# Performance work log

Measured on AMD Instinct MI355X. Metric: run time of the kernel, lower is better.

## Reference

```python
import jax, jax.numpy as jnp
import numpy as np

D_MODEL = 1024
N_HEAD = 16
HEAD_SIZE = D_MODEL // N_HEAD
SEQ = 2048
BATCH = 4
LN_EPS = 1e-5


def layer_norm(x, gamma, beta):
    mu = jnp.mean(x, axis=-1, keepdims=True)
    var = jnp.var(x, axis=-1, keepdims=True)
    return (x - mu) * jax.lax.rsqrt(var + LN_EPS) * gamma + beta


def setup_inputs() -> dict:
    key = jax.random.key(0)
    ks = jax.random.split(key, 12)
    s = 0.02
    return {
        "x": jax.random.normal(ks[0], (BATCH, SEQ, D_MODEL), jnp.float32),
        "Wq": jax.random.normal(ks[1], (N_HEAD, D_MODEL, HEAD_SIZE), jnp.float32) * s,
        "Wk": jax.random.normal(ks[2], (N_HEAD, D_MODEL, HEAD_SIZE), jnp.float32) * s,
        "Wv": jax.random.normal(ks[3], (N_HEAD, D_MODEL, HEAD_SIZE), jnp.float32) * s,
        "Wo": jax.random.normal(ks[4], (D_MODEL, D_MODEL), jnp.float32) * s,
        "bo": jnp.zeros((D_MODEL,), jnp.float32),
        "W1": jax.random.normal(ks[5], (D_MODEL, 4 * D_MODEL), jnp.float32) * s,
        "b1": jnp.zeros((4 * D_MODEL,), jnp.float32),
        "W2": jax.random.normal(ks[6], (4 * D_MODEL, D_MODEL), jnp.float32) * s,
        "b2": jnp.zeros((D_MODEL,), jnp.float32),
        "g1": jnp.ones((D_MODEL,), jnp.float32),
        "be1": jnp.zeros((D_MODEL,), jnp.float32),
        "g2": jnp.ones((D_MODEL,), jnp.float32),
        "be2": jnp.zeros((D_MODEL,), jnp.float32),
    }


def reference(x, Wq, Wk, Wv, Wo, bo, W1, b1, W2, b2, g1, be1, g2, be2):
    B, T, C = x.shape
    # --- self-attention branch (dropout = eval identity) ---
    h = layer_norm(x, g1, be1)
    q = jnp.einsum('btc,hcs->bhts', h, Wq)
    k = jnp.einsum('btc,hcs->bhts', h, Wk)
    v = jnp.einsum('btc,hcs->bhts', h, Wv)
    wei = jnp.einsum('bhts,bhus->bhtu', q, k) * (HEAD_SIZE ** -0.5)
    # non-standard diagonal mask: scores on the diagonal are set to 0 (not -inf)
    diag = jnp.eye(T, dtype=bool)
    wei = jnp.where(diag, jnp.zeros((), wei.dtype), wei)
    wei = jax.nn.softmax(wei, axis=-1)
    att = jnp.einsum('bhtu,bhus->bhts', wei, v)          # [B,H,T,hs]
    att = att.transpose(0, 2, 1, 3).reshape(B, T, C)      # concat heads
    sa = att @ Wo + bo
    x = x + sa
    # --- feed-forward branch ---
    h2 = layer_norm(x, g2, be2)
    ff = jax.nn.gelu(h2 @ W1 + b1, approximate=False) @ W2 + b2
    return x + ff
```

## Files before the change

kernel.cpp:

```cpp
#include <hip/hip_runtime.h>
#include <hip/hip_bf16.h>
#include <math.h>

#define D_MODEL 1024
#define N_HEAD 16
#define HEAD 64
#define SEQ 2048
#define BATCH 4
#define ROWS (BATCH*SEQ)
#define FFD 4096

typedef __bf16 bf16;
typedef __attribute__((ext_vector_type(8))) __bf16 bf16x8;
typedef __attribute__((ext_vector_type(4))) __bf16 bf16x4;
typedef __attribute__((ext_vector_type(4))) float f32x4;
typedef __attribute__((ext_vector_type(16))) float f32x16;
typedef __attribute__((ext_vector_type(4))) short short4v;

static_assert(sizeof(bf16x8) == 16, "bf16x8 must be 16B");

__device__ __forceinline__ void async_copy16(const void* g, void* l) {
  __builtin_amdgcn_global_load_lds((const __attribute__((address_space(1))) void*)g,
                                   (__attribute__((address_space(3))) void*)l, 16, 0, 0);
}

__device__ __forceinline__ f32x4 mfma16(bf16x8 a, bf16x8 b, f32x4 c) {
  return __builtin_amdgcn_mfma_f32_16x16x32_bf16(a, b, c, 0, 0, 0);
}

__device__ __forceinline__ f32x16 mfma32(bf16x8 a, bf16x8 b, f32x16 c) {
  return __builtin_amdgcn_mfma_f32_32x32x16_bf16(a, b, c, 0, 0, 0);
}

__device__ __forceinline__ f32x4 mfma16k16(bf16x4 a, bf16x4 b, f32x4 c) {
#if __has_builtin(__builtin_amdgcn_mfma_f32_16x16x16_bf16)
  return __builtin_amdgcn_mfma_f32_16x16x16_bf16(a, b, c, 0, 0, 0);
#else
  return __builtin_amdgcn_mfma_f32_16x16x16bf16_1k(__builtin_bit_cast(short4v, a),
                                                   __builtin_bit_cast(short4v, b), c, 0, 0, 0);
#endif
}

__device__ __forceinline__ float fast_exp2(float x) {
#if __has_builtin(__builtin_amdgcn_exp2f)
  return __builtin_amdgcn_exp2f(x);
#else
  float r; asm("v_exp_f32 %0, %1" : "=v"(r) : "v"(x)); return r;
#endif
}

__device__ __forceinline__ float fast_gelu(float x) {
  const float y = 0.7978845608f * (x + 0.044715f * x * x * x);
  const float e = fast_exp2(y * 2.88539008178f);
  return 0.5f * x * (1.f + (1.f - 2.f / (e + 1.f)));
}

__global__ __launch_bounds__(256) void transpose_cast_kernel(const float* __restrict__ in,
                                                             bf16* __restrict__ out,
                                                             int R, int C) {
  __shared__ float ts[32][33];
  const int r0 = blockIdx.y * 32, c0 = blockIdx.x * 32;
  const int t = threadIdx.x, lr = t >> 3, lc = (t & 7) * 4;
  const float4 v = *(const float4*)(in + (size_t)(r0 + lr) * C + c0 + lc);
  ts[lr][lc + 0] = v.x; ts[lr][lc + 1] = v.y; ts[lr][lc + 2] = v.z; ts[lr][lc + 3] = v.w;
  __syncthreads();
  bf16x4 o;
  o[0] = (bf16)ts[lc + 0][lr]; o[1] = (bf16)ts[lc + 1][lr];
  o[2] = (bf16)ts[lc + 2][lr]; o[3] = (bf16)ts[lc + 3][lr];
  *(bf16x4*)(out + (size_t)(c0 + lr) * R + r0 + lc) = o;
}

__global__ __launch_bounds__(256) void qkv_transpose_kernel(const float* __restrict__ Wq,
                                                            const float* __restrict__ Wk,
                                                            const float* __restrict__ Wv,
                                                            bf16* __restrict__ out) {
  __shared__ float ts[32][33];
  const int mat = blockIdx.z / N_HEAD, h = blockIdx.z % N_HEAD;
  const float* W = (mat == 0 ? Wq : mat == 1 ? Wk : Wv) + (size_t)h * D_MODEL * HEAD;
  bf16* o = out + (size_t)mat * D_MODEL * D_MODEL + (size_t)(h * HEAD) * D_MODEL;
  const int c0 = blockIdx.x * 32, s0 = blockIdx.y * 32;
  const int t = threadIdx.x, lr = t >> 3, lc = (t & 7) * 4;
  const float4 v = *(const float4*)(W + (size_t)(c0 + lr) * HEAD + s0 + lc);
  ts[lr][lc + 0] = v.x; ts[lr][lc + 1] = v.y; ts[lr][lc + 2] = v.z; ts[lr][lc + 3] = v.w;
  __syncthreads();
  bf16x4 ov;
  ov[0] = (bf16)ts[lc + 0][lr]; ov[1] = (bf16)ts[lc + 1][lr];
  ov[2] = (bf16)ts[lc + 2][lr]; ov[3] = (bf16)ts[lc + 3][lr];
  *(bf16x4*)(o + (size_t)(s0 + lr) * D_MODEL + c0 + lc) = ov;
}

__global__ __launch_bounds__(256) void ln_kernel(const float* __restrict__ x,
                                                 const float* __restrict__ g,
                                                 const float* __restrict__ b,
                                                 bf16* __restrict__ h) {
  const int row = blockIdx.x, t = threadIdx.x;
  const float4 v = *(const float4*)(x + (size_t)row * D_MODEL + t * 4);
  float s = v.x + v.y + v.z + v.w;
  float ss = v.x * v.x + v.y * v.y + v.z * v.z + v.w * v.w;
#pragma unroll
  for (int m = 1; m < 64; m <<= 1) { s += __shfl_xor(s, m); ss += __shfl_xor(ss, m); }
  __shared__ float red[8];
  const int wave = t >> 6, lane = t & 63;
  if (lane == 0) { red[wave] = s; red[4 + wave] = ss; }
  __syncthreads();
  s = red[0] + red[1] + red[2] + red[3];
  ss = red[4] + red[5] + red[6] + red[7];
  const float mu = s * (1.f / D_MODEL);
  const float rstd = rsqrtf(ss * (1.f / D_MODEL) - mu * mu + 1e-5f);
  const float4 gv = *(const float4*)(g + t * 4);
  const float4 bv = *(const float4*)(b + t * 4);
  bf16x4 o;
  o[0] = (bf16)((v.x - mu) * rstd * gv.x + bv.x);
  o[1] = (bf16)((v.y - mu) * rstd * gv.y + bv.y);
  o[2] = (bf16)((v.z - mu) * rstd * gv.z + bv.z);
  o[3] = (bf16)((v.w - mu) * rstd * gv.w + bv.w);
  *(bf16x4*)(h + (size_t)row * D_MODEL + t * 4) = o;
}

template <int EPI>
__global__ __launch_bounds__(256) void gemm_kernel(const bf16* __restrict__ A,
                                                   const bf16* __restrict__ Bt, int K,
                                                   void* __restrict__ outp,
                                                   const float* __restrict__ bias,
                                                   const float* __restrict__ resid,
                                                   bf16* __restrict__ q_out,
                                                   bf16* __restrict__ k_out,
                                                   bf16* __restrict__ vt_out, int N) {
  __shared__ bf16 As[128 * 64];
  __shared__ bf16 Bs[128 * 64];
  const int t = threadIdx.x;
  const int bm = blockIdx.y, bn = blockIdx.x;
  const int srow = t >> 3;
  const int schunk = (t & 7) ^ (srow & 7);
  const bf16* Ag = A + (size_t)(bm * 128 + srow) * K + schunk * 8;
  const bf16* Bg = Bt + (size_t)(bn * 128 + srow) * K + schunk * 8;
  bf16* Asd = As + t * 8;
  bf16* Bsd = Bs + t * 8;

  const int wave = t >> 6, lane = t & 63, l31 = lane & 31, lk = lane >> 5;
  const int wm = (wave >> 1) * 64, wn = (wave & 1) * 64;

  f32x16 acc[2][2];
#pragma unroll
  for (int i = 0; i < 2; i++)
#pragma unroll
    for (int j = 0; j < 2; j++)
#pragma unroll
      for (int e = 0; e < 16; e++) acc[i][j][e] = 0.f;

  for (int kt = 0; kt < K; kt += 64) {
    __syncthreads();
#pragma unroll
    for (int i = 0; i < 4; i++) {
      async_copy16(Ag + kt + (size_t)(32 * i) * K, Asd + 2048 * i);
      async_copy16(Bg + kt + (size_t)(32 * i) * K, Bsd + 2048 * i);
    }
    __syncthreads();
#pragma unroll
    for (int s = 0; s < 4; s++) {
      const int pos = ((s << 1) | lk) ^ (l31 & 7);
      bf16x8 af[2], bfr[2];
#pragma unroll
      for (int i = 0; i < 2; i++) af[i] = *(const bf16x8*)(As + (wm + i * 32 + l31) * 64 + pos * 8);
#pragma unroll
      for (int j = 0; j < 2; j++) bfr[j] = *(const bf16x8*)(Bs + (wn + j * 32 + l31) * 64 + pos * 8);
#pragma unroll
      for (int i = 0; i < 2; i++)
#pragma unroll
        for (int j = 0; j < 2; j++) acc[i][j] = mfma32(af[i], bfr[j], acc[i][j]);
    }
  }

#pragma unroll
  for (int i = 0; i < 2; i++) {
#pragma unroll
    for (int j = 0; j < 2; j++) {
      const int n = bn * 128 + wn + j * 32 + l31;
#pragma unroll
      for (int e = 0; e < 16; e++) {
        const int m = bm * 128 + wm + i * 32 + (e & 3) + 8 * (e >> 2) + 4 * lk;
        float val = acc[i][j][e];
        if constexpr (EPI == 0) {
          const int b = m >> 11, tt = m & 2047;
          if (n < D_MODEL) {
            const int hh = n >> 6, sgl = n & 63;
            q_out[(size_t)((b * N_HEAD + hh) * SEQ + tt) * HEAD + sgl] = (bf16)val;
          } else if (n < 2 * D_MODEL) {
            const int n2 = n - D_MODEL, hh = n2 >> 6, sgl = n2 & 63;
            k_out[(size_t)((b * N_HEAD + hh) * SEQ + tt) * HEAD + sgl] = (bf16)val;
          } else {
            const int n2 = n - 2 * D_MODEL, hh = n2 >> 6, sgl = n2 & 63;
            vt_out[(size_t)((b * N_HEAD + hh) * HEAD + sgl) * SEQ + tt] = (bf16)val;
          }
        } else if constexpr (EPI == 1) {
          ((float*)outp)[(size_t)m * N + n] = val + bias[n] + resid[(size_t)m * N + n];
        } else if constexpr (EPI == 2) {
          ((bf16*)outp)[(size_t)m * N + n] = (bf16)fast_gelu(val + bias[n]);
        } else {
          ((float*)outp)[(size_t)m * N + n] = val + bias[n] + resid[(size_t)m * N + n];
        }
      }
    }
  }
}

__global__ __launch_bounds__(256, 2) void attn_kernel(const bf16* __restrict__ q,
                                                      const bf16* __restrict__ k,
                                                      const bf16* __restrict__ vt,
                                                      bf16* __restrict__ att) {
  __shared__ bf16 Ks[64 * 64];
  __shared__ bf16 Vs[64 * 64];
  const int t = threadIdx.x, wave = t >> 6, lane = t & 63;
  const int l15 = lane & 15, l4 = lane >> 4;
  const int bh = blockIdx.x & 63, qblk = blockIdx.x >> 6;
  const bf16* qb = q + (size_t)bh * SEQ * HEAD;
  const bf16* kb = k + (size_t)bh * SEQ * HEAD;
  const bf16* vb = vt + (size_t)bh * HEAD * SEQ;
  const int qrow = qblk * 256 + wave * 64;

  const int tr = t >> 3, tc = t & 7, sw = tc ^ (tr & 7);
  const bf16* ksrc0 = kb + (size_t)tr * HEAD + sw * 8;
  const bf16* ksrc1 = kb + (size_t)(tr + 32) * HEAD + sw * 8;
  const bf16* vsrc0 = vb + (size_t)tr * SEQ + sw * 8;
  const bf16* vsrc1 = vb + (size_t)(tr + 32) * SEQ + sw * 8;
  bf16* kd0 = Ks + t * 8; bf16* kd1 = Ks + t * 8 + 2048;
  bf16* vd0 = Vs + t * 8; bf16* vd1 = Vs + t * 8 + 2048;

  const float qscale = 0.125f * 1.44269504088896340736f;
  bf16x8 qf[4][2];
#pragma unroll
  for (int qs = 0; qs < 4; qs++)
#pragma unroll
    for (int h = 0; h < 2; h++) {
      const bf16x8 raw = *(const bf16x8*)(qb + (size_t)(qrow + qs * 16 + l15) * HEAD + h * 32 + l4 * 8);
      bf16x8 sc;
#pragma unroll
      for (int e = 0; e < 8; e++) sc[e] = (bf16)((float)raw[e] * qscale);
      qf[qs][h] = sc;
    }

  f32x4 o[4][4];
  float lsum[4] = {0.f, 0.f, 0.f, 0.f};
#pragma unroll
  for (int qs = 0; qs < 4; qs++)
#pragma unroll
    for (int dm = 0; dm < 4; dm++) { f32x4 z = {0.f, 0.f, 0.f, 0.f}; o[qs][dm] = z; }

  const int rsw = l15 & 7;

  for (int u0 = 0; u0 < SEQ; u0 += 64) {
    __syncthreads();
    async_copy16(ksrc0 + (size_t)u0 * HEAD, kd0);
    async_copy16(ksrc1 + (size_t)u0 * HEAD, kd1);
    async_copy16(vsrc0 + u0, vd0);
    async_copy16(vsrc1 + u0, vd1);
    __syncthreads();

    bf16x8 kf[4][2];
#pragma unroll
    for (int n = 0; n < 4; n++)
#pragma unroll
      for (int h = 0; h < 2; h++)
        kf[n][h] = *(const bf16x8*)(Ks + (n * 16 + l15) * 64 + (((h << 2) | l4) ^ rsw) * 8);
    bf16x4 vf[4][4];
#pragma unroll
    for (int dm = 0; dm < 4; dm++)
#pragma unroll
      for (int n = 0; n < 4; n++)
        vf[dm][n] = *(const bf16x4*)(Vs + (dm * 16 + l15) * 64 + ((((n << 1) | (l4 >> 1)) ^ rsw) * 8) + (l4 & 1) * 4);

#pragma unroll
    for (int qs = 0; qs < 4; qs++) {
      f32x4 s[4];
#pragma unroll
      for (int n = 0; n < 4; n++) {
        f32x4 c = {0.f, 0.f, 0.f, 0.f};
        c = mfma16(kf[n][0], qf[qs][0], c);
        c = mfma16(kf[n][1], qf[qs][1], c);
        s[n] = c;
      }
      if (u0 == qrow) {
#pragma unroll
        for (int r = 0; r < 4; r++)
          s[qs][r] = (l15 == l4 * 4 + r) ? 0.f : s[qs][r];
      }
      bf16x4 pf[4];
      float ls = 0.f;
#pragma unroll
      for (int n = 0; n < 4; n++) {
        f32x4 pv;
#pragma unroll
        for (int r = 0; r < 4; r++) { pv[r] = fast_exp2(s[n][r]); ls += pv[r]; }
        bf16x4 pb;
#pragma unroll
        for (int r = 0; r < 4; r++) pb[r] = (bf16)pv[r];
        pf[n] = pb;
      }
      lsum[qs] += ls;
#pragma unroll
      for (int dm = 0; dm < 4; dm++) {
        f32x4 acc = o[qs][dm];
#pragma unroll
        for (int n = 0; n < 4; n++) acc = mfma16k16(vf[dm][n], pf[n], acc);
        o[qs][dm] = acc;
      }
    }
  }

#pragma unroll
  for (int qs = 0; qs < 4; qs++) {
    float l = lsum[qs];
    l += __shfl_xor(l, 16);
    l += __shfl_xor(l, 32);
    lsum[qs] = l;
  }
  const int b = bh >> 4, hh = bh & 15;
#pragma unroll
  for (int qs = 0; qs < 4; qs++) {
    const float linv = 1.0f / lsum[qs];
#pragma unroll
    for (int dm = 0; dm < 4; dm++) {
      bf16x4 ov;
#pragma unroll
      for (int r = 0; r < 4; r++) ov[r] = (bf16)(o[qs][dm][r] * linv);
      *(bf16x4*)(att + (size_t)(b * SEQ + qrow + qs * 16 + l15) * D_MODEL + hh * HEAD + dm * 16 + l4 * 4) = ov;
    }
  }
}

extern "C" void kernel_launch(void* const* d_in, const int* in_sizes, int n_in,
                              void* d_out, int out_size, void* d_ws, size_t ws_size,
                              hipStream_t stream) {
  const float* x   = (const float*)d_in[0];
  const float* Wq  = (const float*)d_in[1];
  const float* Wk  = (const float*)d_in[2];
  const float* Wv  = (const float*)d_in[3];
  const float* Wo  = (const float*)d_in[4];
  const float* bo  = (const float*)d_in[5];
  const float* W1  = (const float*)d_in[6];
  const float* b1  = (const float*)d_in[7];
  const float* W2  = (const float*)d_in[8];
  const float* b2  = (const float*)d_in[9];
  const float* g1  = (const float*)d_in[10];
  const float* be1 = (const float*)d_in[11];
  const float* g2  = (const float*)d_in[12];
  const float* be2 = (const float*)d_in[13];
  float* out = (float*)d_out;

  bf16* Wqkv_t = (bf16*)d_ws;
  bf16* Wo_t   = Wqkv_t + (size_t)3 * D_MODEL * D_MODEL;
  bf16* W1_t   = Wo_t + (size_t)D_MODEL * D_MODEL;
  bf16* W2_t   = W1_t + (size_t)FFD * D_MODEL;
  bf16* hbuf   = W2_t + (size_t)D_MODEL * FFD;
  float* x1    = (float*)(hbuf + (size_t)ROWS * D_MODEL);
  bf16* big    = (bf16*)(x1 + (size_t)ROWS * D_MODEL);
  bf16* qbuf   = big;
  bf16* kbuf   = qbuf + (size_t)ROWS * D_MODEL;
  bf16* vtbuf  = kbuf + (size_t)ROWS * D_MODEL;
  bf16* ffbuf  = big;
  bf16* attb   = big + (size_t)ROWS * FFD;

  qkv_transpose_kernel<<<dim3(D_MODEL / 32, HEAD / 32, 3 * N_HEAD), 256, 0, stream>>>(Wq, Wk, Wv, Wqkv_t);
  transpose_cast_kernel<<<dim3(D_MODEL / 32, D_MODEL / 32), 256, 0, stream>>>(Wo, Wo_t, D_MODEL, D_MODEL);
  transpose_cast_kernel<<<dim3(FFD / 32, D_MODEL / 32), 256, 0, stream>>>(W1, W1_t, D_MODEL, FFD);
  transpose_cast_kernel<<<dim3(D_MODEL / 32, FFD / 32), 256, 0, stream>>>(W2, W2_t, FFD, D_MODEL);
  ln_kernel<<<ROWS, 256, 0, stream>>>(x, g1, be1, hbuf);
  gemm_kernel<0><<<dim3(3 * D_MODEL / 128, ROWS / 128), 256, 0, stream>>>(
      hbuf, Wqkv_t, D_MODEL, nullptr, nullptr, nullptr, qbuf, kbuf, vtbuf, 3 * D_MODEL);
  attn_kernel<<<64 * (SEQ / 256), 256, 0, stream>>>(qbuf, kbuf, vtbuf, attb);
  gemm_kernel<1><<<dim3(D_MODEL / 128, ROWS / 128), 256, 0, stream>>>(
      attb, Wo_t, D_MODEL, x1, bo, x, nullptr, nullptr, nullptr, D_MODEL);
  ln_kernel<<<ROWS, 256, 0, stream>>>(x1, g2, be2, hbuf);
  gemm_kernel<2><<<dim3(FFD / 128, ROWS / 128), 256, 0, stream>>>(
      hbuf, W1_t, D_MODEL, ffbuf, b1, nullptr, nullptr, nullptr, nullptr, FFD);
  gemm_kernel<3><<<dim3(D_MODEL / 128, ROWS / 128), 256, 0, stream>>>(
      ffbuf, W2_t, FFD, out, b2, x1, nullptr, nullptr, nullptr, D_MODEL);
}
```

Before: 535.3 us.

## Merge weight-prep and first layernorm into one launch; halve attention query tile

Replaces four weight transpose/cast launches and the first layernorm launch with a single block-indexed prep kernel, cutting launch overhead and letting those small jobs overlap. The attention kernel now gives each wave 32 query rows instead of 64. That doubles the grid to 1024 blocks and raises the occupancy hint to 3, with the diagonal-mask index adjusted to match. The trade-off is that each K/V tile loaded into LDS is reused by half as many queries, so K/V traffic per query doubles.

```diff
diff --git a/kernel.cpp b/kernel.cpp
--- a/kernel.cpp
+++ b/kernel.cpp
@@ -55,12 +55,65 @@
   return 0.5f * x * (1.f + (1.f - 2.f / (e + 1.f)));
 }
 
-__global__ __launch_bounds__(256) void transpose_cast_kernel(const float* __restrict__ in,
-                                                             bf16* __restrict__ out,
-                                                             int R, int C) {
+__global__ __launch_bounds__(256) void prep_kernel(const float* __restrict__ x,
+                                                   const float* __restrict__ g1,
+                                                   const float* __restrict__ be1,
+                                                   bf16* __restrict__ hbuf,
+                                                   const float* __restrict__ Wq,
+                                                   const float* __restrict__ Wk,
+                                                   const float* __restrict__ Wv,
+                                                   bf16* __restrict__ Wqkv_t,
+                                                   const float* __restrict__ Wo, bf16* __restrict__ Wo_t,
+                                                   const float* __restrict__ W1, bf16* __restrict__ W1_t,
+                                                   const float* __restrict__ W2, bf16* __restrict__ W2_t) {
+  const int b = blockIdx.x, t = threadIdx.x;
+  if (b < 8192) {
+    const int row = b;
+    const float4 v = *(const float4*)(x + (size_t)row * D_MODEL + t * 4);
+    float s = v.x + v.y + v.z + v.w;
+    float ss = v.x * v.x + v.y * v.y + v.z * v.z + v.w * v.w;
+#pragma unroll
+    for (int m = 1; m < 64; m <<= 1) { s += __shfl_xor(s, m); ss += __shfl_xor(ss, m); }
+    __shared__ float red[8];
+    const int wave = t >> 6, lane = t & 63;
+    if (lane == 0) { red[wave] = s; red[4 + wave] = ss; }
+    __syncthreads();
+    s = red[0] + red[1] + red[2] + red[3];
+    ss = red[4] + red[5] + red[6] + red[7];
+    const float mu = s * (1.f / D_MODEL);
+    const float rstd = rsqrtf(ss * (1.f / D_MODEL) - mu * mu + 1e-5f);
+    const float4 gv = *(const float4*)(g1 + t * 4);
+    const float4 bv = *(const float4*)(be1 + t * 4);
+    bf16x4 o;
+    o[0] = (bf16)((v.x - mu) * rstd * gv.x + bv.x);
+    o[1] = (bf16)((v.y - mu) * rstd * gv.y + bv.y);
+    o[2] = (bf16)((v.z - mu) * rstd * gv.z + bv.z);
+    o[3] = (bf16)((v.w - mu) * rstd * gv.w + bv.w);
+    *(bf16x4*)(hbuf + (size_t)row * D_MODEL + t * 4) = o;
+    return;
+  }
   __shared__ float ts[32][33];
-  const int r0 = blockIdx.y * 32, c0 = blockIdx.x * 32;
-  const int t = threadIdx.x, lr = t >> 3, lc = (t & 7) * 4;
+  const float* in; bf16* out; int R, C, r0, c0;
+  if (b < 11264) {
+    const int idx = b - 8192;
+    const int mat = idx >> 10, idx2 = idx & 1023;
+    const int h = idx2 >> 6, rr = idx2 & 63;
+    in = (mat == 0 ? Wq : mat == 1 ? Wk : Wv) + (size_t)h * D_MODEL * HEAD;
+    out = Wqkv_t + (size_t)mat * D_MODEL * D_MODEL + (size_t)(h * HEAD) * D_MODEL;
+    R = D_MODEL; C = HEAD;
+    r0 = (rr >> 1) * 32;
+    c0 = (rr & 1) * 32;
+  } else if (b < 12288) {
+    const int r = b - 11264; in = Wo; out = Wo_t; R = 1024; C = 1024;
+    r0 = (r >> 5) * 32; c0 = (r & 31) * 32;
+  } else if (b < 16384) {
+    const int r = b - 12288; in = W1; out = W1_t; R = 1024; C = 4096;
+    r0 = (r >> 7) * 32; c0 = (r & 127) * 32;
+  } else {
+    const int r = b - 16384; in = W2; out = W2_t; R = 4096; C = 1024;
+    r0 = (r >> 5) * 32; c0 = (r & 31) * 32;
+  }
+  const int lr = t >> 3, lc = (t & 7) * 4;
   const float4 v = *(const float4*)(in + (size_t)(r0 + lr) * C + c0 + lc);
   ts[lr][lc + 0] = v.x; ts[lr][lc + 1] = v.y; ts[lr][lc + 2] = v.z; ts[lr][lc + 3] = v.w;
   __syncthreads();
@@ -68,25 +121,6 @@
   o[0] = (bf16)ts[lc + 0][lr]; o[1] = (bf16)ts[lc + 1][lr];
   o[2] = (bf16)ts[lc + 2][lr]; o[3] = (bf16)ts[lc + 3][lr];
   *(bf16x4*)(out + (size_t)(c0 + lr) * R + r0 + lc) = o;
-}
-
-__global__ __launch_bounds__(256) void qkv_transpose_kernel(const float* __restrict__ Wq,
-                                                            const float* __restrict__ Wk,
-                                                            const float* __restrict__ Wv,
-                                                            bf16* __restrict__ out) {
-  __shared__ float ts[32][33];
-  const int mat = blockIdx.z / N_HEAD, h = blockIdx.z % N_HEAD;
-  const float* W = (mat == 0 ? Wq : mat == 1 ? Wk : Wv) + (size_t)h * D_MODEL * HEAD;
-  bf16* o = out + (size_t)mat * D_MODEL * D_MODEL + (size_t)(h * HEAD) * D_MODEL;
-  const int c0 = blockIdx.x * 32, s0 = blockIdx.y * 32;
-  const int t = threadIdx.x, lr = t >> 3, lc = (t & 7) * 4;
-  const float4 v = *(const float4*)(W + (size_t)(c0 + lr) * HEAD + s0 + lc);
-  ts[lr][lc + 0] = v.x; ts[lr][lc + 1] = v.y; ts[lr][lc + 2] = v.z; ts[lr][lc + 3] = v.w;
-  __syncthreads();
-  bf16x4 ov;
-  ov[0] = (bf16)ts[lc + 0][lr]; ov[1] = (bf16)ts[lc + 1][lr];
-  ov[2] = (bf16)ts[lc + 2][lr]; ov[3] = (bf16)ts[lc + 3][lr];
-  *(bf16x4*)(o + (size_t)(s0 + lr) * D_MODEL + c0 + lc) = ov;
 }
 
 __global__ __launch_bounds__(256) void ln_kernel(const float* __restrict__ x,
@@ -204,7 +238,7 @@
   }
 }
 
-__global__ __launch_bounds__(256, 2) void attn_kernel(const bf16* __restrict__ q,
+__global__ __launch_bounds__(256, 3) void attn_kernel(const bf16* __restrict__ q,
                                                       const bf16* __restrict__ k,
                                                       const bf16* __restrict__ vt,
                                                       bf16* __restrict__ att) {
@@ -216,7 +250,7 @@
   const bf16* qb = q + (size_t)bh * SEQ * HEAD;
   const bf16* kb = k + (size_t)bh * SEQ * HEAD;
   const bf16* vb = vt + (size_t)bh * HEAD * SEQ;
-  const int qrow = qblk * 256 + wave * 64;
+  const int qrow = qblk * 128 + wave * 32;
 
   const int tr = t >> 3, tc = t & 7, sw = tc ^ (tr & 7);
   const bf16* ksrc0 = kb + (size_t)tr * HEAD + sw * 8;
@@ -227,9 +261,9 @@
   bf16* vd0 = Vs + t * 8; bf16* vd1 = Vs + t * 8 + 2048;
 
   const float qscale = 0.125f * 1.44269504088896340736f;
-  bf16x8 qf[4][2];
-#pragma unroll
-  for (int qs = 0; qs < 4; qs++)
+  bf16x8 qf[2][2];
+#pragma unroll
+  for (int qs = 0; qs < 2; qs++)
 #pragma unroll
     for (int h = 0; h < 2; h++) {
       const bf16x8 raw = *(const bf16x8*)(qb + (size_t)(qrow + qs * 16 + l15) * HEAD + h * 32 + l4 * 8);
@@ -239,14 +273,16 @@
       qf[qs][h] = sc;
     }
 
-  f32x4 o[4][4];
-  float lsum[4] = {0.f, 0.f, 0.f, 0.f};
-#pragma unroll
-  for (int qs = 0; qs < 4; qs++)
+  f32x4 o[2][4];
+  float lsum[2] = {0.f, 0.f};
+#pragma unroll
+  for (int qs = 0; qs < 2; qs++)
 #pragma unroll
     for (int dm = 0; dm < 4; dm++) { f32x4 z = {0.f, 0.f, 0.f, 0.f}; o[qs][dm] = z; }
 
   const int rsw = l15 & 7;
+  const int u0d = qrow & ~63;
+  const int ndiag0 = (qrow - u0d) >> 4;
 
   for (int u0 = 0; u0 < SEQ; u0 += 64) {
     __syncthreads();
@@ -270,7 +306,7 @@
         vf[dm][n] = *(const bf16x4*)(Vs + (dm * 16 + l15) * 64 + ((((n << 1) | (l4 >> 1)) ^ rsw) * 8) + (l4 & 1) * 4);
 
 #pragma unroll
-    for (int qs = 0; qs < 4; qs++) {
+    for (int qs = 0; qs < 2; qs++) {
       f32x4 s[4];
 #pragma unroll
       for (int n = 0; n < 4; n++) {
@@ -279,10 +315,11 @@
         c = mfma16(kf[n][1], qf[qs][1], c);
         s[n] = c;
       }
-      if (u0 == qrow) {
+      if (u0 == u0d) {
+        const int nd = ndiag0 + qs;
 #pragma unroll
         for (int r = 0; r < 4; r++)
-          s[qs][r] = (l15 == l4 * 4 + r) ? 0.f : s[qs][r];
+          s[nd][r] = (l15 == l4 * 4 + r) ? 0.f : s[nd][r];
       }
       bf16x4 pf[4];
       float ls = 0.f;
@@ -308,7 +345,7 @@
   }
 
 #pragma unroll
-  for (int qs = 0; qs < 4; qs++) {
+  for (int qs = 0; qs < 2; qs++) {
     float l = lsum[qs];
     l += __shfl_xor(l, 16);
     l += __shfl_xor(l, 32);
@@ -316,7 +353,7 @@
   }
   const int b = bh >> 4, hh = bh & 15;
 #pragma unroll
-  for (int qs = 0; qs < 4; qs++) {
+  for (int qs = 0; qs < 2; qs++) {
     const float linv = 1.0f / lsum[qs];
 #pragma unroll
     for (int dm = 0; dm < 4; dm++) {
@@ -360,14 +397,11 @@
   bf16* ffbuf  = big;
   bf16* attb   = big + (size_t)ROWS * FFD;
 
-  qkv_transpose_kernel<<<dim3(D_MODEL / 32, HEAD / 32, 3 * N_HEAD), 256, 0, stream>>>(Wq, Wk, Wv, Wqkv_t);
-  transpose_cast_kernel<<<dim3(D_MODEL / 32, D_MODEL / 32), 256, 0, stream>>>(Wo, Wo_t, D_MODEL, D_MODEL);
-  transpose_cast_kernel<<<dim3(FFD / 32, D_MODEL / 32), 256, 0, stream>>>(W1, W1_t, D_MODEL, FFD);
-  transpose_cast_kernel<<<dim3(D_MODEL / 32, FFD / 32), 256, 0, stream>>>(W2, W2_t, FFD, D_MODEL);
-  ln_kernel<<<ROWS, 256, 0, stream>>>(x, g1, be1, hbuf);
+  prep_kernel<<<20480, 256, 0, stream>>>(x, g1, be1, hbuf, Wq, Wk, Wv, Wqkv_t,
+                                         Wo, Wo_t, W1, W1_t, W2, W2_t);
   gemm_kernel<0><<<dim3(3 * D_MODEL / 128, ROWS / 128), 256, 0, stream>>>(
       hbuf, Wqkv_t, D_MODEL, nullptr, nullptr, nullptr, qbuf, kbuf, vtbuf, 3 * D_MODEL);
-  attn_kernel<<<64 * (SEQ / 256), 256, 0, stream>>>(qbuf, kbuf, vtbuf, attb);
+  attn_kernel<<<64 * (SEQ / 128), 256, 0, stream>>>(qbuf, kbuf, vtbuf, attb);
   gemm_kernel<1><<<dim3(D_MODEL / 128, ROWS / 128), 256, 0, stream>>>(
       attb, Wo_t, D_MODEL, x1, bo, x, nullptr, nullptr, nullptr, D_MODEL);
   ln_kernel<<<ROWS, 256, 0, stream>>>(x1, g2, be2, hbuf);
```

Measured after the change: 543.8 us. About the same (+1.6%).
